# Kernel optimization log

Hardware: AMD Instinct MI355X
Metric: run time of the kernel (lower is better)

The kernel has to match this reference:

```python
import jax, jax.numpy as jnp
import numpy as np

EPS = 1e-6  # clamp for arccos domain (matches typical GeodesicLoss eps)


def _random_rotations(key, n):
    # Orthonormalize random matrices into proper rotations (stand-in for
    # the gemmi symmetry operators of 'P 61 2 2', S=12 ops).
    A = jax.random.normal(key, (n, 3, 3), dtype=jnp.float32)
    Q, R = jnp.linalg.qr(A)
    # fix signs so det = +1
    d = jnp.sign(jnp.diagonal(R, axis1=-2, axis2=-1))
    Q = Q * d[:, None, :]
    det = jnp.linalg.det(Q)
    Q = Q.at[:, :, 0].multiply(det[:, None])
    return Q


def setup_inputs() -> dict:
    key = jax.random.key(0)
    k1, k2, k3 = jax.random.split(key, 3)
    B, C, S = 32768, 64, 12
    R_pred = _random_rotations(k1, B * C).reshape(B, C, 3, 3)
    R_gt = _random_rotations(k2, B)
    rot_mats = _random_rotations(k3, S)
    return {"R_pred": R_pred, "R_gt": R_gt, "rot_mats": rot_mats}


def reference(R_pred, R_gt, rot_mats):
    # R_gt_sym[b,s] = rot_mats[s] @ R_gt[b]  -> (B, S, 3, 3)
    R_gt_sym = jnp.einsum('sij,bjk->bsik', rot_mats, R_gt)
    # geodesic loss: arccos((trace(R_pred @ R_gt_sym^T) - 1) / 2)
    # trace(A @ B^T) = sum_ij A_ij * B_ij  -> avoids materializing (B,C,S,3,3)
    tr = jnp.einsum('bcij,bsij->bcs', R_pred, R_gt_sym)
    cos = jnp.clip((tr - 1.0) * 0.5, -1.0 + EPS, 1.0 - EPS)
    all_losses = jnp.arccos(cos)            # (B, C, S)
    min_loss_sym = jnp.min(all_losses, axis=2)   # min over symmetry ops
    best_candidate = jnp.min(min_loss_sym, axis=1)  # min over candidates
    return best_candidate.mean()
```

## Files before the change

kernel.cpp:

```cpp
#include <hip/hip_runtime.h>
#include <math.h>

#define EPS_CLIP 1e-6f
#define BPB 4

template <int SS>
__global__ __launch_bounds__(256) void sym_loss_kernel(
    const float* __restrict__ R_pred,
    const float* __restrict__ R_gt,
    const float* __restrict__ rot,
    float* __restrict__ partial,
    int S_rt)
{
    const int S = SS ? SS : S_rt;

    __shared__ float sP[BPB * 64 * 9];
    __shared__ float sLoss[BPB];

    const int tid = threadIdx.x;
    const int b0  = blockIdx.x * BPB;

    const float4* src4 = reinterpret_cast<const float4*>(R_pred + (size_t)b0 * 64 * 9);
    float4* dst4 = reinterpret_cast<float4*>(sP);
    #pragma unroll
    for (int i = 0; i < 3; ++i) {
        const int idx = tid + i * 256;
        if (idx < BPB * 64 * 9 / 4) dst4[idx] = src4[idx];
    }
    __syncthreads();

    const int c  = tid & 63;
    const int bi = tid >> 6;
    const int b  = b0 + bi;

    float p[9];
    const float* Pp = sP + (bi * 64 + c) * 9;
    #pragma unroll
    for (int e = 0; e < 9; ++e) p[e] = Pp[e];

    const float* G = R_gt + (size_t)b * 9;
    float g[9];
    #pragma unroll
    for (int e = 0; e < 9; ++e) g[e] = G[e];

    float q[9];
    #pragma unroll
    for (int i = 0; i < 3; ++i)
        #pragma unroll
        for (int j = 0; j < 3; ++j)
            q[i * 3 + j] = fmaf(p[i * 3 + 0], g[j * 3 + 0],
                           fmaf(p[i * 3 + 1], g[j * 3 + 1],
                                p[i * 3 + 2] * g[j * 3 + 2]));

    float m = -1e30f;
    #pragma unroll
    for (int s = 0; s < (SS ? SS : 1) * (SS ? 1 : 1); ++s) { }
    if (SS) {
        #pragma unroll
        for (int s = 0; s < SS; ++s) {
            const float* Rs = rot + s * 9;
            float tr = 0.f;
            #pragma unroll
            for (int e = 0; e < 9; ++e) tr = fmaf(q[e], Rs[e], tr);
            m = fmaxf(m, tr);
        }
    } else {
        for (int s = 0; s < S; ++s) {
            const float* Rs = rot + s * 9;
            float tr = 0.f;
            #pragma unroll
            for (int e = 0; e < 9; ++e) tr = fmaf(q[e], Rs[e], tr);
            m = fmaxf(m, tr);
        }
    }

    #pragma unroll
    for (int off = 32; off; off >>= 1) m = fmaxf(m, __shfl_xor(m, off));

    if (c == 0) {
        float cosv = (m - 1.0f) * 0.5f;
        cosv = fminf(fmaxf(cosv, -1.0f + EPS_CLIP), 1.0f - EPS_CLIP);
        sLoss[bi] = acosf(cosv);
    }
    __syncthreads();

    if (tid == 0) {
        float sum = 0.f;
        #pragma unroll
        for (int i = 0; i < BPB; ++i) sum += sLoss[i];
        partial[blockIdx.x] = sum;
    }
}

__global__ __launch_bounds__(1024) void reduce_kernel(
    const float* __restrict__ partial, int n, float* __restrict__ out, float invB)
{
    float sum = 0.f;
    for (int i = threadIdx.x; i < n; i += 1024) sum += partial[i];
    #pragma unroll
    for (int off = 32; off; off >>= 1) sum += __shfl_xor(sum, off);
    __shared__ float ws[16];
    const int w = threadIdx.x >> 6;
    if ((threadIdx.x & 63) == 0) ws[w] = sum;
    __syncthreads();
    if (threadIdx.x == 0) {
        float t = 0.f;
        #pragma unroll
        for (int i = 0; i < 16; ++i) t += ws[i];
        out[0] = t * invB;
    }
}

extern "C" void kernel_launch(void* const* d_in, const int* in_sizes, int n_in,
                              void* d_out, int out_size, void* d_ws, size_t ws_size,
                              hipStream_t stream) {
    const float* R_pred = (const float*)d_in[0];
    const float* R_gt   = (const float*)d_in[1];
    const float* rot    = (const float*)d_in[2];
    float* out = (float*)d_out;

    const int B = in_sizes[1] / 9;
    const int S = in_sizes[2] / 9;
    const int nblocks = B / BPB;

    float* partial = (float*)d_ws;

    if (S == 12)
        sym_loss_kernel<12><<<nblocks, 256, 0, stream>>>(R_pred, R_gt, rot, partial, S);
    else
        sym_loss_kernel<0><<<nblocks, 256, 0, stream>>>(R_pred, R_gt, rot, partial, S);

    reduce_kernel<<<1, 1024, 0, stream>>>(partial, nblocks, out, 1.0f / (float)B);
}
```

Measured before the change: 25.40 us.

## Process multiple batch tiles per block with register-prefetched double-buffered LDS

Each block now handles four 4-batch tiles in sequence. While the current tile is computed out of one LDS buffer, the next tile's R_pred data is prefetched into registers, so global load latency overlaps compute. The per-batch R_gt index is made wave-uniform via readfirstlane so the loads can become scalar, and the final reduce kernel shrinks to 256 threads over four times fewer partials. The cost is fewer blocks (2048) and therefore less parallelism on a memory-bound kernel, plus higher register and LDS use per block.

```diff
diff --git a/kernel.cpp b/kernel.cpp
--- a/kernel.cpp
+++ b/kernel.cpp
@@ -3,6 +3,8 @@
 
 #define EPS_CLIP 1e-6f
 #define BPB 4
+#define TILES 4
+#define NF4 (BPB * 64 * 9 / 4)
 
 template <int SS>
 __global__ __launch_bounds__(256) void sym_loss_kernel(
@@ -10,78 +12,103 @@
     const float* __restrict__ R_gt,
     const float* __restrict__ rot,
     float* __restrict__ partial,
-    int S_rt)
+    int S_rt, int nTiles)
 {
     const int S = SS ? SS : S_rt;
 
-    __shared__ float sP[BPB * 64 * 9];
+    __shared__ float sP[2][BPB * 64 * 9];
     __shared__ float sLoss[BPB];
 
     const int tid = threadIdx.x;
-    const int b0  = blockIdx.x * BPB;
+    const int c   = tid & 63;
+    const int bi  = tid >> 6;
+    const int t0  = blockIdx.x * TILES;
 
-    const float4* src4 = reinterpret_cast<const float4*>(R_pred + (size_t)b0 * 64 * 9);
-    float4* dst4 = reinterpret_cast<float4*>(sP);
-    #pragma unroll
-    for (int i = 0; i < 3; ++i) {
-        const int idx = tid + i * 256;
-        if (idx < BPB * 64 * 9 / 4) dst4[idx] = src4[idx];
-    }
-    __syncthreads();
+    const float4* src4 = reinterpret_cast<const float4*>(R_pred);
 
-    const int c  = tid & 63;
-    const int bi = tid >> 6;
-    const int b  = b0 + bi;
-
-    float p[9];
-    const float* Pp = sP + (bi * 64 + c) * 9;
-    #pragma unroll
-    for (int e = 0; e < 9; ++e) p[e] = Pp[e];
-
-    const float* G = R_gt + (size_t)b * 9;
-    float g[9];
-    #pragma unroll
-    for (int e = 0; e < 9; ++e) g[e] = G[e];
-
-    float q[9];
-    #pragma unroll
-    for (int i = 0; i < 3; ++i)
-        #pragma unroll
-        for (int j = 0; j < 3; ++j)
-            q[i * 3 + j] = fmaf(p[i * 3 + 0], g[j * 3 + 0],
-                           fmaf(p[i * 3 + 1], g[j * 3 + 1],
-                                p[i * 3 + 2] * g[j * 3 + 2]));
-
-    float m = -1e30f;
-    #pragma unroll
-    for (int s = 0; s < (SS ? SS : 1) * (SS ? 1 : 1); ++s) { }
-    if (SS) {
-        #pragma unroll
-        for (int s = 0; s < SS; ++s) {
-            const float* Rs = rot + s * 9;
-            float tr = 0.f;
-            #pragma unroll
-            for (int e = 0; e < 9; ++e) tr = fmaf(q[e], Rs[e], tr);
-            m = fmaxf(m, tr);
-        }
-    } else {
-        for (int s = 0; s < S; ++s) {
-            const float* Rs = rot + s * 9;
-            float tr = 0.f;
-            #pragma unroll
-            for (int e = 0; e < 9; ++e) tr = fmaf(q[e], Rs[e], tr);
-            m = fmaxf(m, tr);
-        }
+    float4 r0, r1, r2;
+    {
+        const size_t base = (size_t)t0 * NF4;
+        r0 = src4[base + tid];
+        r1 = src4[base + tid + 256];
+        if (tid < NF4 - 512) r2 = src4[base + tid + 512];
     }
 
+    float lsum = 0.f;
+    int buf = 0;
+
     #pragma unroll
-    for (int off = 32; off; off >>= 1) m = fmaxf(m, __shfl_xor(m, off));
+    for (int k = 0; k < TILES; ++k) {
+        const int t = t0 + k;
 
-    if (c == 0) {
-        float cosv = (m - 1.0f) * 0.5f;
-        cosv = fminf(fmaxf(cosv, -1.0f + EPS_CLIP), 1.0f - EPS_CLIP);
-        sLoss[bi] = acosf(cosv);
+        float4* dst4 = reinterpret_cast<float4*>(sP[buf]);
+        dst4[tid]       = r0;
+        dst4[tid + 256] = r1;
+        if (tid < NF4 - 512) dst4[tid + 512] = r2;
+        __syncthreads();
+
+        if (k + 1 < TILES && t + 1 < nTiles) {
+            const size_t base = (size_t)(t + 1) * NF4;
+            r0 = src4[base + tid];
+            r1 = src4[base + tid + 256];
+            if (tid < NF4 - 512) r2 = src4[base + tid + 512];
+        }
+
+        const int b = t * BPB + bi;
+
+        float p[9];
+        const float* Pp = sP[buf] + (bi * 64 + c) * 9;
+        #pragma unroll
+        for (int e = 0; e < 9; ++e) p[e] = Pp[e];
+
+        const int bu = __builtin_amdgcn_readfirstlane(b);
+        const float* G = R_gt + (size_t)bu * 9;
+        float g[9];
+        #pragma unroll
+        for (int e = 0; e < 9; ++e) g[e] = G[e];
+
+        float q[9];
+        #pragma unroll
+        for (int i = 0; i < 3; ++i)
+            #pragma unroll
+            for (int j = 0; j < 3; ++j)
+                q[i * 3 + j] = fmaf(p[i * 3 + 0], g[j * 3 + 0],
+                               fmaf(p[i * 3 + 1], g[j * 3 + 1],
+                                    p[i * 3 + 2] * g[j * 3 + 2]));
+
+        float m = -1e30f;
+        if (SS) {
+            #pragma unroll
+            for (int s = 0; s < SS; ++s) {
+                const float* Rs = rot + s * 9;
+                float tr = 0.f;
+                #pragma unroll
+                for (int e = 0; e < 9; ++e) tr = fmaf(q[e], Rs[e], tr);
+                m = fmaxf(m, tr);
+            }
+        } else {
+            for (int s = 0; s < S; ++s) {
+                const float* Rs = rot + s * 9;
+                float tr = 0.f;
+                #pragma unroll
+                for (int e = 0; e < 9; ++e) tr = fmaf(q[e], Rs[e], tr);
+                m = fmaxf(m, tr);
+            }
+        }
+
+        #pragma unroll
+        for (int off = 32; off; off >>= 1) m = fmaxf(m, __shfl_xor(m, off));
+
+        if (c == 0) {
+            float cosv = (m - 1.0f) * 0.5f;
+            cosv = fminf(fmaxf(cosv, -1.0f + EPS_CLIP), 1.0f - EPS_CLIP);
+            lsum += acosf(cosv);
+        }
+
+        buf ^= 1;
     }
+
+    if (c == 0) sLoss[bi] = lsum;
     __syncthreads();
 
     if (tid == 0) {
@@ -92,23 +119,18 @@
     }
 }
 
-__global__ __launch_bounds__(1024) void reduce_kernel(
+__global__ __launch_bounds__(256) void reduce_kernel(
     const float* __restrict__ partial, int n, float* __restrict__ out, float invB)
 {
     float sum = 0.f;
-    for (int i = threadIdx.x; i < n; i += 1024) sum += partial[i];
+    for (int i = threadIdx.x; i < n; i += 256) sum += partial[i];
     #pragma unroll
     for (int off = 32; off; off >>= 1) sum += __shfl_xor(sum, off);
-    __shared__ float ws[16];
+    __shared__ float ws[4];
     const int w = threadIdx.x >> 6;
     if ((threadIdx.x & 63) == 0) ws[w] = sum;
     __syncthreads();
-    if (threadIdx.x == 0) {
-        float t = 0.f;
-        #pragma unroll
-        for (int i = 0; i < 16; ++i) t += ws[i];
-        out[0] = t * invB;
-    }
+    if (threadIdx.x == 0) out[0] = (ws[0] + ws[1] + ws[2] + ws[3]) * invB;
 }
 
 extern "C" void kernel_launch(void* const* d_in, const int* in_sizes, int n_in,
@@ -121,14 +143,15 @@
 
     const int B = in_sizes[1] / 9;
     const int S = in_sizes[2] / 9;
-    const int nblocks = B / BPB;
+    const int nTiles  = B / BPB;
+    const int nBlocks = (nTiles + TILES - 1) / TILES;
 
     float* partial = (float*)d_ws;
 
     if (S == 12)
-        sym_loss_kernel<12><<<nblocks, 256, 0, stream>>>(R_pred, R_gt, rot, partial, S);
+        sym_loss_kernel<12><<<nBlocks, 256, 0, stream>>>(R_pred, R_gt, rot, partial, S, nTiles);
     else
-        sym_loss_kernel<0><<<nblocks, 256, 0, stream>>>(R_pred, R_gt, rot, partial, S);
+        sym_loss_kernel<0><<<nBlocks, 256, 0, stream>>>(R_pred, R_gt, rot, partial, S, nTiles);
 
-    reduce_kernel<<<1, 1024, 0, stream>>>(partial, nblocks, out, 1.0f / (float)B);
+    reduce_kernel<<<1, 256, 0, stream>>>(partial, nBlocks, out, 1.0f / (float)B);
 }
```

New measurement: 24.51 us. 1.04x faster.

## Process four batches per wave with register prefetch instead of LDS staging

Applied to the files above, without the earlier changes.

Drops the shared-memory staging of R_pred and the barrier that followed it. Each wave now handles four batch entries in turn, loading each lane's 3x3 matrix straight into registers and prefetching the next entry's matrix while computing the current one. Lane 0 accumulates the per-wave losses, and the grid shrinks by a factor of four, so there are fewer blocks and partials. The cost is lower parallelism (2048 blocks) and non-coalesced 12-byte loads per lane.

```diff
diff --git a/kernel.cpp b/kernel.cpp
--- a/kernel.cpp
+++ b/kernel.cpp
@@ -2,7 +2,10 @@
 #include <math.h>
 
 #define EPS_CLIP 1e-6f
-#define BPB 4
+#define WPB 4
+#define NWAVES 4
+
+struct F3 { float x, y, z; };
 
 template <int SS>
 __global__ __launch_bounds__(256) void sym_loss_kernel(
@@ -12,82 +15,83 @@
     float* __restrict__ partial,
     int S_rt)
 {
-    const int S = SS ? SS : S_rt;
+    const int S    = SS ? SS : S_rt;
+    const int tid  = threadIdx.x;
+    const int lane = tid & 63;
+    const int wid  = tid >> 6;
+    const int gw   = __builtin_amdgcn_readfirstlane(blockIdx.x * NWAVES + wid);
+    const int b0   = gw * WPB;
 
-    __shared__ float sP[BPB * 64 * 9];
-    __shared__ float sLoss[BPB];
+    F3 a0, a1, a2;
+    {
+        const F3* src = reinterpret_cast<const F3*>(R_pred + ((size_t)b0 * 64 + lane) * 9);
+        a0 = src[0]; a1 = src[1]; a2 = src[2];
+    }
 
-    const int tid = threadIdx.x;
-    const int b0  = blockIdx.x * BPB;
+    float lsum = 0.f;
 
-    const float4* src4 = reinterpret_cast<const float4*>(R_pred + (size_t)b0 * 64 * 9);
-    float4* dst4 = reinterpret_cast<float4*>(sP);
     #pragma unroll
-    for (int i = 0; i < 3; ++i) {
-        const int idx = tid + i * 256;
-        if (idx < BPB * 64 * 9 / 4) dst4[idx] = src4[idx];
-    }
-    __syncthreads();
+    for (int k = 0; k < WPB; ++k) {
+        const int b = __builtin_amdgcn_readfirstlane(b0 + k);
 
-    const int c  = tid & 63;
-    const int bi = tid >> 6;
-    const int b  = b0 + bi;
+        float p[9] = { a0.x, a0.y, a0.z, a1.x, a1.y, a1.z, a2.x, a2.y, a2.z };
 
-    float p[9];
-    const float* Pp = sP + (bi * 64 + c) * 9;
-    #pragma unroll
-    for (int e = 0; e < 9; ++e) p[e] = Pp[e];
+        if (k + 1 < WPB) {
+            const F3* src = reinterpret_cast<const F3*>(R_pred + ((size_t)(b + 1) * 64 + lane) * 9);
+            a0 = src[0]; a1 = src[1]; a2 = src[2];
+        }
 
-    const float* G = R_gt + (size_t)b * 9;
-    float g[9];
-    #pragma unroll
-    for (int e = 0; e < 9; ++e) g[e] = G[e];
+        const float* G = R_gt + (size_t)b * 9;
+        float g[9];
+        #pragma unroll
+        for (int e = 0; e < 9; ++e) g[e] = G[e];
 
-    float q[9];
-    #pragma unroll
-    for (int i = 0; i < 3; ++i)
+        float q[9];
         #pragma unroll
-        for (int j = 0; j < 3; ++j)
-            q[i * 3 + j] = fmaf(p[i * 3 + 0], g[j * 3 + 0],
-                           fmaf(p[i * 3 + 1], g[j * 3 + 1],
-                                p[i * 3 + 2] * g[j * 3 + 2]));
+        for (int i = 0; i < 3; ++i)
+            #pragma unroll
+            for (int j = 0; j < 3; ++j)
+                q[i * 3 + j] = fmaf(p[i * 3 + 0], g[j * 3 + 0],
+                               fmaf(p[i * 3 + 1], g[j * 3 + 1],
+                                    p[i * 3 + 2] * g[j * 3 + 2]));
 
-    float m = -1e30f;
-    #pragma unroll
-    for (int s = 0; s < (SS ? SS : 1) * (SS ? 1 : 1); ++s) { }
-    if (SS) {
+        float m = -1e30f;
+        if (SS) {
+            #pragma unroll
+            for (int s = 0; s < SS; ++s) {
+                const float* Rs = rot + s * 9;
+                float tr = 0.f;
+                #pragma unroll
+                for (int e = 0; e < 9; ++e) tr = fmaf(q[e], Rs[e], tr);
+                m = fmaxf(m, tr);
+            }
+        } else {
+            for (int s = 0; s < S; ++s) {
+                const float* Rs = rot + s * 9;
+                float tr = 0.f;
+                #pragma unroll
+                for (int e = 0; e < 9; ++e) tr = fmaf(q[e], Rs[e], tr);
+                m = fmaxf(m, tr);
+            }
+        }
+
         #pragma unroll
-        for (int s = 0; s < SS; ++s) {
-            const float* Rs = rot + s * 9;
-            float tr = 0.f;
-            #pragma unroll
-            for (int e = 0; e < 9; ++e) tr = fmaf(q[e], Rs[e], tr);
-            m = fmaxf(m, tr);
-        }
-    } else {
-        for (int s = 0; s < S; ++s) {
-            const float* Rs = rot + s * 9;
-            float tr = 0.f;
-            #pragma unroll
-            for (int e = 0; e < 9; ++e) tr = fmaf(q[e], Rs[e], tr);
-            m = fmaxf(m, tr);
+        for (int off = 32; off; off >>= 1) m = fmaxf(m, __shfl_xor(m, off));
+
+        if (lane == 0) {
+            float cosv = (m - 1.0f) * 0.5f;
+            cosv = fminf(fmaxf(cosv, -1.0f + EPS_CLIP), 1.0f - EPS_CLIP);
+            lsum += acosf(cosv);
         }
     }
 
-    #pragma unroll
-    for (int off = 32; off; off >>= 1) m = fmaxf(m, __shfl_xor(m, off));
-
-    if (c == 0) {
-        float cosv = (m - 1.0f) * 0.5f;
-        cosv = fminf(fmaxf(cosv, -1.0f + EPS_CLIP), 1.0f - EPS_CLIP);
-        sLoss[bi] = acosf(cosv);
-    }
+    __shared__ float sLoss[NWAVES];
+    if (lane == 0) sLoss[wid] = lsum;
     __syncthreads();
-
     if (tid == 0) {
         float sum = 0.f;
         #pragma unroll
-        for (int i = 0; i < BPB; ++i) sum += sLoss[i];
+        for (int i = 0; i < NWAVES; ++i) sum += sLoss[i];
         partial[blockIdx.x] = sum;
     }
 }
@@ -121,14 +125,14 @@
 
     const int B = in_sizes[1] / 9;
     const int S = in_sizes[2] / 9;
-    const int nblocks = B / BPB;
+    const int nBlocks = B / (WPB * NWAVES);
 
     float* partial = (float*)d_ws;
 
     if (S == 12)
-        sym_loss_kernel<12><<<nblocks, 256, 0, stream>>>(R_pred, R_gt, rot, partial, S);
+        sym_loss_kernel<12><<<nBlocks, 256, 0, stream>>>(R_pred, R_gt, rot, partial, S);
     else
-        sym_loss_kernel<0><<<nblocks, 256, 0, stream>>>(R_pred, R_gt, rot, partial, S);
+        sym_loss_kernel<0><<<nBlocks, 256, 0, stream>>>(R_pred, R_gt, rot, partial, S);
 
-    reduce_kernel<<<1, 1024, 0, stream>>>(partial, nblocks, out, 1.0f / (float)B);
+    reduce_kernel<<<1, 1024, 0, stream>>>(partial, nBlocks, out, 1.0f / (float)B);
 }
```

Measured after the change: 21.37 us. 1.19x faster.
